# Kernel optimization log

Measured on AMD Instinct MI355X. Metric: run time of the kernel, lower is better.

## Reference

```python
import jax, jax.numpy as jnp
import numpy as np

T, D, H, N = 2048, 2048, 32, 64
DW, DA, DV, DG = 64, 64, 32, 128


def _ln(x, w, b, eps):
    mu = x.mean(-1, keepdims=True)
    var = ((x - mu) ** 2).mean(-1, keepdims=True)
    return (x - mu) * jax.lax.rsqrt(var + eps) * w + b


def setup_inputs() -> dict:
    key = jax.random.key(0)
    ks = iter(jax.random.split(key, 40))

    def rn(shape, s=0.02):
        return jax.random.normal(next(ks), shape, dtype=jnp.float32) * s

    def ru(shape):
        return jax.random.uniform(next(ks), shape, dtype=jnp.float32)

    return dict(
        x=rn((T, D), 1.0),
        state1=rn((1, D), 1.0),
        state2=rn((H, N, N), 0.1),
        v_first=rn((T, D), 1.0),
        ln1_w=jnp.ones((D,), jnp.float32),
        ln1_b=jnp.zeros((D,), jnp.float32),
        x_r=ru((D,)), x_w=ru((D,)), x_k=ru((D,)),
        x_v=ru((D,)), x_a=ru((D,)), x_g=ru((D,)),
        W_r=rn((D, D)), W_k=rn((D, D)), W_v=rn((D, D)), W_o=rn((D, D)),
        w1=rn((D, DW)), w2=rn((DW, D)), w0=rn((D,), 0.5),
        a1=rn((D, DA)), a2=rn((DA, D)), a0=rn((D,), 0.5),
        v1=rn((D, DV)), v2=rn((DV, D)), v0=rn((D,), 0.5),
        g1=rn((D, DG)), g2=rn((DG, D)),
        k_k=rn((D,), 0.5), k_a=rn((D,), 0.5), r_k=rn((D,), 0.5),
        ln_x_w=jnp.ones((D,), jnp.float32),
        ln_x_b=jnp.zeros((D,), jnp.float32),
    )


def reference(x, state1, state2, v_first, ln1_w, ln1_b,
              x_r, x_w, x_k, x_v, x_a, x_g,
              W_r, W_k, W_v, W_o,
              w1, w2, w0, a1, a2, a0, v1, v2, v0, g1, g2,
              k_k, k_a, r_k, ln_x_w, ln_x_b):
    # ln1 + token shift
    xn = _ln(x, ln1_w, ln1_b, 1e-5)                      # [T, D]
    sx = jnp.concatenate([state1, xn[:-1]], axis=0) - xn  # shifted - x
    xr = xn + sx * x_r
    xw = xn + sx * x_w
    xk = xn + sx * x_k
    xv = xn + sx * x_v
    xa = xn + sx * x_a
    xg = xn + sx * x_g

    r = xr @ W_r.T
    # decay: w = exp(-0.606531 * sigmoid(w0 + tanh(xw@w1)@w2))
    w = jnp.exp(-0.606531 * jax.nn.sigmoid(jnp.tanh(xw @ w1) @ w2 + w0))
    k = xk @ W_k.T
    v = xv @ W_v.T
    a = jax.nn.sigmoid(xa @ a1 @ a2 + a0)
    g = jax.nn.sigmoid(xg @ g1) @ g2
    # layer_id != 0: blend with v_first via v-lora
    v = v + (v_first - v) * jax.nn.sigmoid(xv @ v1 @ v2 + v0)

    kh = (k * k_k).reshape(T, H, N)
    kk = kh / (jnp.linalg.norm(kh, axis=-1, keepdims=True) + 1e-6)  # l2norm per head
    k = k * (1.0 + (a - 1.0) * k_a)

    rh = r.reshape(T, H, N)
    wh = w.reshape(T, H, N)
    khh = k.reshape(T, H, N)
    vh = v.reshape(T, H, N)
    ab = kk * a.reshape(T, H, N)  # b input to wkv

    def step(S, t):
        r_t, w_t, k_t, v_t, kk_t, ab_t = t
        sa = jnp.einsum('hij,hj->hi', S, -kk_t)  # state @ a (a = -kk column)
        S = (S * w_t[:, None, :]
             + sa[:, :, None] * ab_t[:, None, :]
             + v_t[:, :, None] * k_t[:, None, :])
        return S, jnp.einsum('hij,hj->hi', S, r_t)

    state2_out, xo = jax.lax.scan(step, state2, (rh, wh, khh, vh, kk, ab))  # xo: [T,H,N]

    # per-head layernorm (ln_x, eps=0.00064), then full-width affine
    xo = _ln(xo, jnp.float32(1.0), jnp.float32(0.0), 0.00064)
    xo = xo.reshape(T, D) * ln_x_w + ln_x_b
    # r_k bonus term
    bonus = ((rh * khh * r_k.reshape(H, N)).sum(-1, keepdims=True) * vh).reshape(T, D)
    xo = (xo + bonus) * g
    out = x + xo @ W_o.T
    return out, xn[-1:], state2_out
```

## Files before the change

### kernel.cpp

```cpp
#include <hip/hip_runtime.h>

#define Tn 2048
#define Dn 2048
#define Hn 32
#define Cn 32
#define NCH (Tn / Cn)

typedef float f32x4 __attribute__((ext_vector_type(4)));
typedef __bf16 bf16x8 __attribute__((ext_vector_type(8)));
typedef __bf16 bf16x4 __attribute__((ext_vector_type(4)));

template <int CTRL>
__device__ __forceinline__ float dpp_add(float x) {
  int xi = __builtin_bit_cast(int, x);
  int sh = __builtin_amdgcn_update_dpp(0, xi, CTRL, 0xf, 0xf, true);
  return x + __builtin_bit_cast(float, sh);
}
__device__ __forceinline__ float rdlane(float x, int l) {
  int xi = __builtin_bit_cast(int, x);
  return __builtin_bit_cast(float, __builtin_amdgcn_readlane(xi, l));
}
__device__ __forceinline__ float waveSum(float v) {
  v = dpp_add<0x111>(v);
  v = dpp_add<0x112>(v);
  v = dpp_add<0x114>(v);
  v = dpp_add<0x118>(v);
  return (rdlane(v, 15) + rdlane(v, 31)) + (rdlane(v, 47) + rdlane(v, 63));
}

__device__ __forceinline__ float sigm(float x) { return 1.f / (1.f + expf(-x)); }

__device__ __forceinline__ void gl_lds16(const void* g, void* l) {
  __builtin_amdgcn_global_load_lds(
      (__attribute__((address_space(1))) void*)(g),
      (__attribute__((address_space(3))) void*)(l), 16, 0, 0);
}

__device__ __forceinline__ void bar_lgkm() {
  asm volatile("s_waitcnt lgkmcnt(0)" ::: "memory");
  __builtin_amdgcn_s_barrier();
}

__device__ __forceinline__ f32x4 mfma16(const __bf16* a, const __bf16* b, f32x4 acc) {
  return __builtin_amdgcn_mfma_f32_16x16x32_bf16(
      *(const bf16x8*)a, *(const bf16x8*)b, acc, 0, 0, 0);
}


__global__ __launch_bounds__(256) void castw3_kernel(
    const float* __restrict__ A, const float* __restrict__ B,
    const float* __restrict__ C, __bf16* __restrict__ o0,
    __bf16* __restrict__ o1, __bf16* __restrict__ o2) {
  const int z = blockIdx.y;
  const float* src = z == 0 ? A : (z == 1 ? B : C);
  __bf16* dst = z == 0 ? o0 : (z == 1 ? o1 : o2);
  const size_t i4 = (size_t)blockIdx.x * 256 + threadIdx.x;
  f32x4 v = *(const f32x4*)(src + i4 * 4);
  bf16x4 o;
  o[0] = (__bf16)v[0]; o[1] = (__bf16)v[1]; o[2] = (__bf16)v[2]; o[3] = (__bf16)v[3];
  ((bf16x4*)dst)[i4] = o;
}

__global__ __launch_bounds__(256) void cast1_kernel(
    const float* __restrict__ src, __bf16* __restrict__ dst) {
  const size_t i4 = (size_t)blockIdx.x * 256 + threadIdx.x;
  f32x4 v = *(const f32x4*)(src + i4 * 4);
  bf16x4 o;
  o[0] = (__bf16)v[0]; o[1] = (__bf16)v[1]; o[2] = (__bf16)v[2]; o[3] = (__bf16)v[3];
  ((bf16x4*)dst)[i4] = o;
}

__global__ __launch_bounds__(256) void castT_kernel(
    const float* __restrict__ w2, const float* __restrict__ a2,
    const float* __restrict__ v2, const float* __restrict__ g2,
    __bf16* __restrict__ w2T, __bf16* __restrict__ a2T,
    __bf16* __restrict__ v2T, __bf16* __restrict__ g2T) {
  const int i = blockIdx.x;
  const int k = threadIdx.x;
  if (k < 128) {
    w2T[(size_t)i * 128 + k] = (k < 64) ? (__bf16)w2[(size_t)k * Dn + i] : (__bf16)0.f;
    a2T[(size_t)i * 128 + k] = (k < 64) ? (__bf16)a2[(size_t)k * Dn + i] : (__bf16)0.f;
    v2T[(size_t)i * 128 + k] = (k < 32) ? (__bf16)v2[(size_t)k * Dn + i] : (__bf16)0.f;
    g2T[(size_t)i * 128 + k] = (__bf16)g2[(size_t)k * Dn + i];
  }
}

__global__ __launch_bounds__(256) void castU_kernel(
    const float* __restrict__ w1, const float* __restrict__ a1,
    const float* __restrict__ v1, const float* __restrict__ g1,
    __bf16* __restrict__ uwT, __bf16* __restrict__ uaT,
    __bf16* __restrict__ uvT, __bf16* __restrict__ ugT) {
  const int z = blockIdx.y;
  const float* src = z == 0 ? w1 : (z == 1 ? a1 : (z == 2 ? v1 : g1));
  __bf16* dst = z == 0 ? uwT : (z == 1 ? uaT : (z == 2 ? uvT : ugT));
  const int R = z == 0 ? 64 : (z == 1 ? 64 : (z == 2 ? 32 : 128));
  const int d = blockIdx.x;
  const int k = threadIdx.x;
  if (k < 128)
    dst[(size_t)k * Dn + d] = (k < R) ? (__bf16)src[(size_t)d * R + k] : (__bf16)0.f;
}


__global__ __launch_bounds__(256) void ln_kernel(
    const float* __restrict__ x, const float* __restrict__ lw,
    const float* __restrict__ lb, __bf16* __restrict__ xn,
    float* __restrict__ xn_last) {
  __shared__ float red[8];
  const int t = blockIdx.x, tid = threadIdx.x;
  const int lane = tid & 63, wv = tid >> 6;
  const float* xr = x + (size_t)t * Dn;
  float v[8];
  float s = 0.f;
#pragma unroll
  for (int c = 0; c < 8; ++c) { v[c] = xr[tid + c * 256]; s += v[c]; }
  s = waveSum(s);
  if (lane == 0) red[wv] = s;
  __syncthreads();
  const float mu = (red[0] + red[1] + red[2] + red[3]) * (1.f / (float)Dn);
  float q = 0.f;
#pragma unroll
  for (int c = 0; c < 8; ++c) { float d0 = v[c] - mu; q += d0 * d0; }
  q = waveSum(q);
  if (lane == 0) red[4 + wv] = q;
  __syncthreads();
  const float var = (red[4] + red[5] + red[6] + red[7]) * (1.f / (float)Dn);
  const float rstd = rsqrtf(var + 1e-5f);
#pragma unroll
  for (int c = 0; c < 8; ++c) {
    const int d = tid + c * 256;
    const float y = (v[c] - mu) * rstd * lw[d] + lb[d];
    xn[(size_t)t * Dn + d] = (__bf16)y;
    if (t == Tn - 1) xn_last[d] = y;
  }
}


__global__ __launch_bounds__(256) void mix_kernel(
    const __bf16* __restrict__ xn, const float* __restrict__ state1,
    const float* __restrict__ cr, const float* __restrict__ cw,
    const float* __restrict__ ck, const float* __restrict__ cv,
    const float* __restrict__ ca, const float* __restrict__ cg,
    __bf16* __restrict__ br, __bf16* __restrict__ bw, __bf16* __restrict__ bk,
    __bf16* __restrict__ bv, __bf16* __restrict__ ba, __bf16* __restrict__ bg) {
  const size_t i4 = (size_t)blockIdx.x * 256 + threadIdx.x;
  const int t = (int)(i4 >> 9);
  const int d = (int)(i4 & 511) * 4;
  const bf16x4 cb = ((const bf16x4*)xn)[i4];
  f32x4 cur;
#pragma unroll
  for (int e = 0; e < 4; ++e) cur[e] = (float)cb[e];
  f32x4 prv;
  if (t == 0) {
    prv = *(const f32x4*)(state1 + d);
  } else {
    const bf16x4 pb = ((const bf16x4*)xn)[i4 - 512];
#pragma unroll
    for (int e = 0; e < 4; ++e) prv[e] = (float)pb[e];
  }
  const f32x4 sx = prv - cur;
  auto mix1 = [&](const float* c, __bf16* o) {
    const f32x4 cc = *(const f32x4*)(c + d);
    bf16x4 ob;
#pragma unroll
    for (int e = 0; e < 4; ++e) ob[e] = (__bf16)(cur[e] + sx[e] * cc[e]);
    ((bf16x4*)o)[i4] = ob;
  };
  mix1(cr, br); mix1(cw, bw); mix1(ck, bk);
  mix1(cv, bv); mix1(ca, ba); mix1(cg, bg);
}


__device__ __forceinline__ void gemm_tile(const __bf16* __restrict__ A,
                                          const __bf16* __restrict__ B,
                                          int K, int row0, int col0,
                                          f32x4 (&acc)[4][4]) {
  __shared__ __attribute__((aligned(16))) __bf16 As[4096];
  __shared__ __attribute__((aligned(16))) __bf16 Bs[4096];
  const int tid = threadIdx.x;
  const int lane = tid & 63, wid = tid >> 6;
  const int wm = (wid >> 1) * 64, wn = (wid & 1) * 64;
  const int lr = lane & 15, lk = (lane >> 4) * 8;
  for (int kt = 0; kt < K; kt += 32) {
#pragma unroll
    for (int it = 0; it < 2; ++it) {
      const int L = it * 256 + tid;
      const int rr = L >> 2, kc = (L & 3) * 8;
      const int lb = (it * 256 + wid * 64) * 8;
      gl_lds16(A + (size_t)(row0 + rr) * K + (kt + kc), &As[lb]);
      gl_lds16(B + (size_t)(col0 + rr) * K + (kt + kc), &Bs[lb]);
    }
    __syncthreads();
    bf16x8 af[4], bfv[4];
#pragma unroll
    for (int mf = 0; mf < 4; ++mf)
      af[mf] = *(const bf16x8*)&As[(wm + mf * 16 + lr) * 32 + lk];
#pragma unroll
    for (int nf = 0; nf < 4; ++nf)
      bfv[nf] = *(const bf16x8*)&Bs[(wn + nf * 16 + lr) * 32 + lk];
#pragma unroll
    for (int mf = 0; mf < 4; ++mf)
#pragma unroll
      for (int nf = 0; nf < 4; ++nf)
        acc[mf][nf] = __builtin_amdgcn_mfma_f32_16x16x32_bf16(
            af[mf], bfv[nf], acc[mf][nf], 0, 0, 0);
    __syncthreads();
  }
}

__global__ __launch_bounds__(256) void gemm37_kernel(
    const __bf16* __restrict__ A0, const __bf16* __restrict__ A1,
    const __bf16* __restrict__ A2, const __bf16* __restrict__ B0,
    const __bf16* __restrict__ B1, const __bf16* __restrict__ B2,
    __bf16* __restrict__ C0, __bf16* __restrict__ C1, __bf16* __restrict__ C2,
    const __bf16* __restrict__ Aw, const __bf16* __restrict__ Aa,
    const __bf16* __restrict__ Av, const __bf16* __restrict__ Ag,
    const __bf16* __restrict__ Bw, const __bf16* __restrict__ Ba,
    const __bf16* __restrict__ Bv, const __bf16* __restrict__ Bg,
    __bf16* __restrict__ Cw, __bf16* __restrict__ Ca,
    __bf16* __restrict__ Cv, __bf16* __restrict__ Cg) {
  const int z = blockIdx.z;
  if (z >= 3 && blockIdx.y != 0) return;
  const __bf16* A; const __bf16* B; __bf16* C;
  switch (z) {
    case 0: A = A0; B = B0; C = C0; break;
    case 1: A = A1; B = B1; C = C1; break;
    case 2: A = A2; B = B2; C = C2; break;
    case 3: A = Aw; B = Bw; C = Cw; break;
    case 4: A = Aa; B = Ba; C = Ca; break;
    case 5: A = Av; B = Bv; C = Cv; break;
    default: A = Ag; B = Bg; C = Cg; break;
  }
  const int row0 = blockIdx.x * 128, col0 = (z < 3) ? blockIdx.y * 128 : 0;
  const int ldc = (z < 3) ? Dn : 128;
  f32x4 acc[4][4] = {};
  gemm_tile(A, B, Dn, row0, col0, acc);
  const int lane = threadIdx.x & 63, wid = threadIdx.x >> 6;
  const int wm = (wid >> 1) * 64, wn = (wid & 1) * 64;
#pragma unroll
  for (int mf = 0; mf < 4; ++mf) {
    const int r0 = row0 + wm + mf * 16 + ((lane >> 4) << 2);
#pragma unroll
    for (int nf = 0; nf < 4; ++nf) {
      const int c0 = col0 + wn + nf * 16 + (lane & 15);
#pragma unroll
      for (int rg = 0; rg < 4; ++rg) {
        float val = acc[mf][nf][rg];
        if (z == 3)      val = tanhf(val);
        else if (z == 6) val = sigm(val);
        C[(size_t)(r0 + rg) * ldc + c0] = (__bf16)val;
      }
    }
  }
}

__global__ __launch_bounds__(256) void gemm_s2_kernel(
    const __bf16* __restrict__ Aw, const __bf16* __restrict__ Aa,
    const __bf16* __restrict__ Av, const __bf16* __restrict__ Ag,
    const __bf16* __restrict__ Bw, const __bf16* __restrict__ Ba,
    const __bf16* __restrict__ Bv, const __bf16* __restrict__ Bg,
    const float* __restrict__ w0, const float* __restrict__ a0,
    const float* __restrict__ v0, __bf16* __restrict__ Cw,
    __bf16* __restrict__ Ca, __bf16* __restrict__ Cv, __bf16* __restrict__ Cg) {
  const int z = blockIdx.z;
  const __bf16* A = z == 0 ? Aw : (z == 1 ? Aa : (z == 2 ? Av : Ag));
  const __bf16* B = z == 0 ? Bw : (z == 1 ? Ba : (z == 2 ? Bv : Bg));
  const float* bias = z == 0 ? w0 : (z == 1 ? a0 : (z == 2 ? v0 : (const float*)0));
  __bf16* C = z == 0 ? Cw : (z == 1 ? Ca : (z == 2 ? Cv : Cg));
  const int row0 = blockIdx.x * 128, col0 = blockIdx.y * 128;
  f32x4 acc[4][4] = {};
  gemm_tile(A, B, 128, row0, col0, acc);
  const int lane = threadIdx.x & 63, wid = threadIdx.x >> 6;
  const int wm = (wid >> 1) * 64, wn = (wid & 1) * 64;
#pragma unroll
  for (int mf = 0; mf < 4; ++mf) {
    const int r0 = row0 + wm + mf * 16 + ((lane >> 4) << 2);
#pragma unroll
    for (int nf = 0; nf < 4; ++nf) {
      const int c0 = col0 + wn + nf * 16 + (lane & 15);
#pragma unroll
      for (int rg = 0; rg < 4; ++rg) {
        float val = acc[mf][nf][rg];
        if (z == 0)      val = expf(-0.606531f * sigm(val + bias[c0]));
        else if (z < 3)  val = sigm(val + bias[c0]);
        C[(size_t)(r0 + rg) * Dn + c0] = (__bf16)val;
      }
    }
  }
}

__global__ __launch_bounds__(256) void gemm_wo_kernel(
    const __bf16* __restrict__ A, const __bf16* __restrict__ B,
    const float* __restrict__ xres, float* __restrict__ C) {
  const int row0 = blockIdx.x * 128, col0 = blockIdx.y * 128;
  f32x4 acc[4][4] = {};
  gemm_tile(A, B, Dn, row0, col0, acc);
  const int lane = threadIdx.x & 63, wid = threadIdx.x >> 6;
  const int wm = (wid >> 1) * 64, wn = (wid & 1) * 64;
#pragma unroll
  for (int mf = 0; mf < 4; ++mf) {
    const int r0 = row0 + wm + mf * 16 + ((lane >> 4) << 2);
#pragma unroll
    for (int nf = 0; nf < 4; ++nf) {
      const int c0 = col0 + wn + nf * 16 + (lane & 15);
#pragma unroll
      for (int rg = 0; rg < 4; ++rg)
        C[(size_t)(r0 + rg) * Dn + c0] =
            acc[mf][nf][rg] + xres[(size_t)(r0 + rg) * Dn + c0];
    }
  }
}


__global__ __launch_bounds__(256) void prep_kernel(
    const __bf16* __restrict__ r, __bf16* __restrict__ k, __bf16* __restrict__ v,
    const __bf16* __restrict__ a, const __bf16* __restrict__ vb,
    const float* __restrict__ v_first, const float* __restrict__ k_k,
    const float* __restrict__ k_a, const float* __restrict__ r_k,
    __bf16* __restrict__ kk_out, __bf16* __restrict__ ab_out,
    float* __restrict__ dot_out) {
  const int t = blockIdx.x;
  const int lane = threadIdx.x & 63, wv = threadIdx.x >> 6;
#pragma unroll 1
  for (int c = 0; c < 8; ++c) {
    const int d = c * 256 + wv * 64 + lane;
    const size_t idx = (size_t)t * Dn + d;
    const float kvv = (float)k[idx];
    const float kh = kvv * k_k[d];
    const float nrm = sqrtf(waveSum(kh * kh)) + 1e-6f;
    const float kkv = kh / nrm;
    const float av = (float)a[idx];
    float vv = (float)v[idx];
    vv = vv + (v_first[idx] - vv) * (float)vb[idx];
    const float kfv = kvv * (1.f + (av - 1.f) * k_a[d]);
    const float dt = waveSum((float)r[idx] * kfv * r_k[d]);
    kk_out[idx] = (__bf16)kkv;
    ab_out[idx] = (__bf16)(kkv * av);
    k[idx] = (__bf16)kfv;
    v[idx] = (__bf16)vv;
    if (lane == 0) dot_out[t * Hn + (d >> 6)] = dt;
  }
}


__global__ __launch_bounds__(256) void chunkA_kernel(
    const __bf16* __restrict__ wd, const __bf16* __restrict__ kk,
    const __bf16* __restrict__ ab, const __bf16* __restrict__ kf,
    const __bf16* __restrict__ r,
    __bf16* __restrict__ PAg, __bf16* __restrict__ Rtil,
    __bf16* __restrict__ BhatT, __bf16* __restrict__ KhatT,
    __bf16* __restrict__ PKg,
    __bf16* __restrict__ Gbg, __bf16* __restrict__ Gkg,
    float* __restrict__ WCg) {
  const int c = blockIdx.x, h = blockIdx.y;
  const int tid = threadIdx.x;
  const int lane = tid & 63, wid = tid >> 6;
  const int lr = lane & 15, lg = lane >> 4, lk = lg * 8;
  __shared__ __attribute__((aligned(16))) __bf16 A_l[32][72];
  __shared__ __attribute__((aligned(16))) __bf16 B_l[32][72], K_l[32][72], R_l[32][72];
  __shared__ __attribute__((aligned(16))) __bf16 At_t[64][40];
  __shared__ float W_l[33][64];
  __shared__ __attribute__((aligned(16))) __bf16 Mn[32][40], Mt[32][40], Mkat[32][40];
  __shared__ __attribute__((aligned(16))) __bf16 Pa[32][40], Pb[32][40];
  __shared__ __attribute__((aligned(16))) __bf16 Tn_[32][40], Tt_[32][40];
  __shared__ __attribute__((aligned(16))) __bf16 Un_[32][40], Ut_[32][40];

  const size_t rowbase = (size_t)(c * Cn) * Dn + (size_t)h * 64;
  const int tt = tid >> 3, j0 = (tid & 7) * 8;
  const size_t g = rowbase + (size_t)tt * Dn + j0;
  *(bf16x8*)&A_l[tt][j0] = *(const bf16x8*)(wd + g);
  __syncthreads();
  if (tid < 64) {
    const int j = tid;
    float cur = 1.f;
    W_l[0][j] = 1.f;
    for (int t = 0; t < Cn; ++t) {
      cur *= (float)A_l[t][j];
      W_l[t + 1][j] = cur;
    }
    WCg[((size_t)c * Hn + h) * 64 + j] = cur;
  }
  __syncthreads();
  {
    bf16x8 kkv = *(const bf16x8*)(kk + g);
    bf16x8 abv = *(const bf16x8*)(ab + g);
    bf16x8 kv  = *(const bf16x8*)(kf + g);
    bf16x8 rv  = *(const bf16x8*)(r + g);
    bf16x8 oa, ob, ok, orr;
    const size_t tb = ((size_t)c * Hn + h) * 2048;
#pragma unroll
    for (int e = 0; e < 8; ++e) {
      const int j = j0 + e;
      const float Wexc = W_l[tt][j], Winc = W_l[tt + 1][j], WC = W_l[32][j];
      const float inv = 1.f / Winc;
      const float at = -(float)kkv[e] * Wexc;
      const float bt = (float)abv[e] * inv;
      const float kt = (float)kv[e] * inv;
      const float rt = (float)rv[e] * Winc;
      oa[e] = (__bf16)at; ob[e] = (__bf16)bt; ok[e] = (__bf16)kt;
      orr[e] = (__bf16)rt;
      At_t[j][tt] = (__bf16)at;
      BhatT[tb + (size_t)j * 32 + tt] = (__bf16)(bt * WC);
      KhatT[tb + (size_t)j * 32 + tt] = (__bf16)(kt * WC);
    }
    *(bf16x8*)&A_l[tt][j0] = oa;
    *(bf16x8*)&B_l[tt][j0] = ob;
    *(bf16x8*)&K_l[tt][j0] = ok;
    *(bf16x8*)&R_l[tt][j0] = orr;
    *(bf16x8*)(Rtil + g) = orr;
  }
  __syncthreads();
  const size_t matbase = ((size_t)c * Hn + h) * (Cn * Cn);
  {
    const __bf16 (*Ax)[72] = (wid < 2) ? A_l : R_l;
    const __bf16 (*Bx)[72] = ((wid & 1) == 0) ? B_l : K_l;
#pragma unroll
    for (int tile = 0; tile < 4; ++tile) {
      const int tm = (tile >> 1) * 16, tn = (tile & 1) * 16;
      f32x4 acc = {};
      acc = mfma16(&Ax[tm + lr][lk], &Bx[tn + lr][lk], acc);
      acc = mfma16(&Ax[tm + lr][32 + lk], &Bx[tn + lr][32 + lk], acc);
      const int col = tn + lr;
#pragma unroll
      for (int e = 0; e < 4; ++e) {
        const int row = tm + lg * 4 + e;
        if (wid == 0) {
          const __bf16 v = (__bf16)((col < row) ? acc[e] : 0.f);
          Mn[row][col] = v; Mt[col][row] = v;
        } else if (wid == 1) {
          Mkat[col][row] = (__bf16)((col < row) ? acc[e] : 0.f);
        } else if (wid == 2) {
          Gbg[matbase + row * 32 + col] = (__bf16)((col <= row) ? acc[e] : 0.f);
        } else {
          Gkg[matbase + row * 32 + col] = (__bf16)((col <= row) ? acc[e] : 0.f);
        }
      }
    }
  }
  __syncthreads();
  for (int rep = 0; rep < 4; ++rep) {
    const int id = rep * 256 + tid;
    const int t = id >> 5, ta = id & 31;
    Pa[t][ta] = (__bf16)((float)Mn[t][ta] + (t == ta ? 1.f : 0.f));
  }
  __syncthreads();
  const int tm = (wid >> 1) * 16, tn = (wid & 1) * 16;
  auto sq = [&](__bf16 (*Dn_)[40], __bf16 (*Dt_)[40],
                __bf16 (*Xn)[40], __bf16 (*Xt)[40]) {
    f32x4 acc = {};
    acc = mfma16(&Xn[tm + lr][lk], &Xt[tn + lr][lk], acc);
    const int col = tn + lr;
#pragma unroll
    for (int e = 0; e < 4; ++e) {
      const int row = tm + lg * 4 + e;
      const __bf16 v = (__bf16)acc[e];
      Dn_[row][col] = v; Dt_[col][row] = v;
    }
    __syncthreads();
  };
  auto pup = [&](__bf16 (*Dn_)[40], __bf16 (*Pn)[40], __bf16 (*Tt)[40]) {
    f32x4 acc;
    const int col = tn + lr;
#pragma unroll
    for (int e = 0; e < 4; ++e) acc[e] = (float)Pn[tm + lg * 4 + e][col];
    acc = mfma16(&Pn[tm + lr][lk], &Tt[tn + lr][lk], acc);
#pragma unroll
    for (int e = 0; e < 4; ++e) Dn_[tm + lg * 4 + e][col] = (__bf16)acc[e];
    __syncthreads();
  };
  sq(Tn_, Tt_, Mn, Mt);
  pup(Pb, Pa, Tt_);
  sq(Un_, Ut_, Tn_, Tt_);
  pup(Pa, Pb, Ut_);
  sq(Tn_, Tt_, Un_, Ut_);
  pup(Pb, Pa, Tt_);
  sq(Un_, Ut_, Tn_, Tt_);
  pup(Pa, Pb, Ut_);
  {
    f32x4 acc = {};
    acc = mfma16(&Pa[tm + lr][lk], &Mkat[tn + lr][lk], acc);
    const int col = tn + lr;
#pragma unroll
    for (int e = 0; e < 4; ++e)
      PKg[matbase + (tm + lg * 4 + e) * 32 + col] = (__bf16)acc[e];
  }
#pragma unroll
  for (int half = 0; half < 2; ++half) {
    const int jn = (wid & 1) * 16 + half * 32;
    f32x4 acc = {};
    acc = mfma16(&Pa[tm + lr][lk], &At_t[jn + lr][lk], acc);
    const int col = jn + lr;
#pragma unroll
    for (int e = 0; e < 4; ++e)
      PAg[rowbase + (size_t)(tm + lg * 4 + e) * Dn + col] = (__bf16)acc[e];
  }
}


__global__ __launch_bounds__(256) void vt_kernel(
    const __bf16* __restrict__ vbuf, __bf16* __restrict__ Vt) {
  const int c = blockIdx.x, h = blockIdx.y;
  __shared__ __bf16 tile[32][72];
  const int tid = threadIdx.x;
  {
    const int t = tid >> 3, i0 = (tid & 7) * 8;
    *(bf16x8*)&tile[t][i0] =
        *(const bf16x8*)(vbuf + (size_t)(c * Cn + t) * Dn + h * 64 + i0);
  }
  __syncthreads();
  {
    const int i = tid >> 2, t0 = (tid & 3) * 8;
    bf16x8 o;
#pragma unroll
    for (int e = 0; e < 8; ++e) o[e] = tile[t0 + e][i];
    *(bf16x8*)(Vt + ((size_t)c * Hn + h) * 2048 + (size_t)i * 32 + t0) = o;
  }
}


__global__ __launch_bounds__(256) void chunkB_kernel(
    const __bf16* __restrict__ PAg, const __bf16* __restrict__ Rtil,
    const __bf16* __restrict__ BhatT, const __bf16* __restrict__ KhatT,
    const __bf16* __restrict__ PKg,
    const __bf16* __restrict__ Gbg, const __bf16* __restrict__ Gkg,
    const float* __restrict__ WCg, const __bf16* __restrict__ Vt,
    const float* __restrict__ st_in, __bf16* __restrict__ xo,
    float* __restrict__ st_out) {
  const int b = blockIdx.x;
  const int xcd = b & 7, rest = b >> 3;
  const int h = xcd * 4 + (rest & 3);
  const int io = (rest >> 2) * 32;
  const int tid = threadIdx.x;
  const int lane = tid & 63, wid = tid >> 6;
  const int lr = lane & 15, lg = lane >> 4;
  const int lk = lg * 8;

  __shared__ __attribute__((aligned(16))) float S_l[32][68];
  __shared__ __attribute__((aligned(16))) __bf16 Sb_l[32][72];
  __shared__ __attribute__((aligned(16))) __bf16 PA_l[32][72], R_l[32][72];
  __shared__ __attribute__((aligned(16))) __bf16 BhT_l[64][40], KhT_l[64][40];
  __shared__ __attribute__((aligned(16))) __bf16 Vt_l[32][40];
  __shared__ __attribute__((aligned(16))) __bf16 PK_l[32][40];
  __shared__ __attribute__((aligned(16))) __bf16 Gb_l[32][40], Gk_l[32][40];
  __shared__ __attribute__((aligned(16))) __bf16 SA_l[32][40];
  __shared__ float WC_l[64];

  {
    const int i = tid >> 3, j0 = (tid & 7) * 8;
    const float* src = st_in + (size_t)h * 4096 + (size_t)(io + i) * 64 + j0;
    *(f32x4*)&S_l[i][j0] = *(const f32x4*)src;
    *(f32x4*)&S_l[i][j0 + 4] = *(const f32x4*)(src + 4);
  }

  bf16x8 rPA, rR, rBh, rKh;
  bf16x4 rV, rPK, rGb, rGk;
  float rWC = 0.f;

  auto load_regs = [&](int c) {
    const size_t rb = (size_t)(c * Cn) * Dn + (size_t)h * 64;
    {
      const int t = tid >> 3, j0 = (tid & 7) * 8;
      rPA = *(const bf16x8*)(PAg + rb + (size_t)t * Dn + j0);
      rR  = *(const bf16x8*)(Rtil + rb + (size_t)t * Dn + j0);
    }
    const size_t tb = ((size_t)c * Hn + h) * 2048;
    {
      const int jj = tid >> 2, t0 = (tid & 3) * 8;
      rBh = *(const bf16x8*)(BhatT + tb + (size_t)jj * 32 + t0);
      rKh = *(const bf16x8*)(KhatT + tb + (size_t)jj * 32 + t0);
    }
    {
      const int i = tid >> 3, t0 = (tid & 7) * 4;
      rV = *(const bf16x4*)(Vt + tb + (size_t)(io + i) * 32 + t0);
    }
    const size_t mb = ((size_t)c * Hn + h) * 1024 + (size_t)tid * 4;
    rPK = *(const bf16x4*)(PKg + mb);
    rGb = *(const bf16x4*)(Gbg + mb);
    rGk = *(const bf16x4*)(Gkg + mb);
    if (tid < 64) rWC = WCg[((size_t)c * Hn + h) * 64 + tid];
  };
  auto store_lds = [&]() {
    {
      const int t = tid >> 3, j0 = (tid & 7) * 8;
      *(bf16x8*)&PA_l[t][j0] = rPA;
      *(bf16x8*)&R_l[t][j0] = rR;
    }
    {
      const int jj = tid >> 2, t0 = (tid & 3) * 8;
      *(bf16x8*)&BhT_l[jj][t0] = rBh;
      *(bf16x8*)&KhT_l[jj][t0] = rKh;
    }
    {
      const int i = tid >> 3, t0 = (tid & 7) * 4;
      *(bf16x4*)&Vt_l[i][t0] = rV;
    }
    {
      const int t = tid >> 3, u0 = (tid & 7) * 4;
      *(bf16x4*)&PK_l[t][u0] = rPK;
      *(bf16x4*)&Gb_l[t][u0] = rGb;
      *(bf16x4*)&Gk_l[t][u0] = rGk;
    }
    if (tid < 64) WC_l[tid] = rWC;
  };
  auto sb_refresh = [&]() {
    const int i = tid >> 3, j0 = (tid & 7) * 8;
    bf16x8 o;
#pragma unroll
    for (int e = 0; e < 8; ++e) o[e] = (__bf16)S_l[i][j0 + e];
    *(bf16x8*)&Sb_l[i][j0] = o;
  };

  load_regs(0);
  store_lds();
  sb_refresh();
  bar_lgkm();

  const int tm = (wid >> 1) * 16, tn = (wid & 1) * 16;

#pragma unroll 1
  for (int c = 0; c < NCH; ++c) {
    load_regs(c + 1 < NCH ? c + 1 : c);
    {
      f32x4 acc = {};
      acc = mfma16(&PA_l[tm + lr][lk], &Sb_l[tn + lr][lk], acc);
      acc = mfma16(&PA_l[tm + lr][32 + lk], &Sb_l[tn + lr][32 + lk], acc);
      acc = mfma16(&PK_l[tm + lr][lk], &Vt_l[tn + lr][lk], acc);
      bf16x4 o;
#pragma unroll
      for (int e = 0; e < 4; ++e) o[e] = (__bf16)acc[e];
      *(bf16x4*)&SA_l[tn + lr][tm + lg * 4] = o;
    }
    bar_lgkm();
    {
      f32x4 acc = {};
      acc = mfma16(&Gb_l[tm + lr][lk], &SA_l[tn + lr][lk], acc);
      acc = mfma16(&Gk_l[tm + lr][lk], &Vt_l[tn + lr][lk], acc);
      acc = mfma16(&R_l[tm + lr][lk], &Sb_l[tn + lr][lk], acc);
      acc = mfma16(&R_l[tm + lr][32 + lk], &Sb_l[tn + lr][32 + lk], acc);
      const int ig = h * 64 + io + tn + lr;
#pragma unroll
      for (int e = 0; e < 4; ++e)
        xo[(size_t)(c * Cn + tm + lg * 4 + e) * Dn + ig] = (__bf16)acc[e];
    }
#pragma unroll
    for (int tt = 0; tt < 2; ++tt) {
      const int tix = wid + tt * 4;
      const int im = (tix & 1) * 16, jn = (tix >> 1) * 16;
      const float wc = WC_l[jn + lr];
      f32x4 acc;
#pragma unroll
      for (int e = 0; e < 4; ++e) acc[e] = S_l[im + lg * 4 + e][jn + lr] * wc;
      acc = mfma16(&SA_l[im + lr][lk], &BhT_l[jn + lr][lk], acc);
      acc = mfma16(&Vt_l[im + lr][lk], &KhT_l[jn + lr][lk], acc);
#pragma unroll
      for (int e = 0; e < 4; ++e) S_l[im + lg * 4 + e][jn + lr] = acc[e];
    }
    bar_lgkm();
    store_lds();
    sb_refresh();
    bar_lgkm();
  }
  {
    const int i = tid >> 3, j0 = (tid & 7) * 8;
    float* dst = st_out + (size_t)h * 4096 + (size_t)(io + i) * 64 + j0;
    *(f32x4*)dst = *(const f32x4*)&S_l[i][j0];
    *(f32x4*)(dst + 4) = *(const f32x4*)&S_l[i][j0 + 4];
  }
}


__global__ __launch_bounds__(256) void post_kernel(
    const __bf16* __restrict__ xo, const __bf16* __restrict__ v,
    const __bf16* __restrict__ g, const float* __restrict__ dot,
    const float* __restrict__ lnw, const float* __restrict__ lnb,
    __bf16* __restrict__ out) {
  const int t = blockIdx.x;
  const int lane = threadIdx.x & 63, wv = threadIdx.x >> 6;
#pragma unroll 1
  for (int c = 0; c < 8; ++c) {
    const int d = c * 256 + wv * 64 + lane;
    const size_t idx = (size_t)t * Dn + d;
    const float val = (float)xo[idx];
    const float mu = waveSum(val) * (1.f / 64.f);
    const float ctr = val - mu;
    const float var = waveSum(ctr * ctr) * (1.f / 64.f);
    float y = ctr * rsqrtf(var + 0.00064f);
    y = y * lnw[d] + lnb[d];
    const float res = (y + dot[t * Hn + (d >> 6)] * (float)v[idx]) * (float)g[idx];
    out[idx] = (__bf16)res;
  }
}


extern "C" void kernel_launch(void* const* d_in, const int* in_sizes, int n_in,
                              void* d_out, int out_size, void* d_ws, size_t ws_size,
                              hipStream_t stream) {
  (void)in_sizes; (void)n_in; (void)out_size; (void)ws_size;
  const float* x       = (const float*)d_in[0];
  const float* state1  = (const float*)d_in[1];
  const float* state2  = (const float*)d_in[2];
  const float* v_first = (const float*)d_in[3];
  const float* ln1_w   = (const float*)d_in[4];
  const float* ln1_b   = (const float*)d_in[5];
  const float* x_r     = (const float*)d_in[6];
  const float* x_w     = (const float*)d_in[7];
  const float* x_k     = (const float*)d_in[8];
  const float* x_v     = (const float*)d_in[9];
  const float* x_a     = (const float*)d_in[10];
  const float* x_g     = (const float*)d_in[11];
  const float* W_r     = (const float*)d_in[12];
  const float* W_k     = (const float*)d_in[13];
  const float* W_v     = (const float*)d_in[14];
  const float* W_o     = (const float*)d_in[15];
  const float* w1      = (const float*)d_in[16];
  const float* w2      = (const float*)d_in[17];
  const float* w0      = (const float*)d_in[18];
  const float* a1      = (const float*)d_in[19];
  const float* a2      = (const float*)d_in[20];
  const float* a0      = (const float*)d_in[21];
  const float* v1      = (const float*)d_in[22];
  const float* v2      = (const float*)d_in[23];
  const float* v0      = (const float*)d_in[24];
  const float* g1      = (const float*)d_in[25];
  const float* g2      = (const float*)d_in[26];
  const float* k_k     = (const float*)d_in[27];
  const float* k_a     = (const float*)d_in[28];
  const float* r_k     = (const float*)d_in[29];
  const float* lnx_w   = (const float*)d_in[30];
  const float* lnx_b   = (const float*)d_in[31];

  char* p = (char*)d_ws;
  const size_t MB = 1ull << 20;
  __bf16* xn    = (__bf16*)(p + 0 * MB);
  __bf16* PAg   = (__bf16*)(p + 0 * MB);
  __bf16* xr_b  = (__bf16*)(p + 8 * MB);
  __bf16* Wo_b  = (__bf16*)(p + 8 * MB);
  __bf16* xw_b  = (__bf16*)(p + 16 * MB);
  __bf16* wdec  = (__bf16*)(p + 16 * MB);
  __bf16* xo_b  = (__bf16*)(p + 16 * MB);
  __bf16* xk_b  = (__bf16*)(p + 24 * MB);
  __bf16* abuf  = (__bf16*)(p + 24 * MB);
  __bf16* Rtil  = (__bf16*)(p + 24 * MB);
  __bf16* xv_b  = (__bf16*)(p + 32 * MB);
  __bf16* vbl   = (__bf16*)(p + 32 * MB);
  __bf16* BhatT = (__bf16*)(p + 32 * MB);
  __bf16* xa_b  = (__bf16*)(p + 40 * MB);
  __bf16* gbuf  = (__bf16*)(p + 40 * MB);
  __bf16* xg_b  = (__bf16*)(p + 48 * MB);
  __bf16* kkbuf = (__bf16*)(p + 48 * MB);
  __bf16* xobuf = (__bf16*)(p + 48 * MB);
  __bf16* Wr_b  = (__bf16*)(p + 56 * MB);
  __bf16* abbuf = (__bf16*)(p + 56 * MB);
  __bf16* Wk_b  = (__bf16*)(p + 64 * MB);
  __bf16* KhatT = (__bf16*)(p + 64 * MB);
  __bf16* Wv_b  = (__bf16*)(p + 72 * MB);
  __bf16* PKg   = (__bf16*)(p + 72 * MB);
  __bf16* rbuf  = (__bf16*)(p + 80 * MB);
  __bf16* kbuf  = (__bf16*)(p + 88 * MB);
  __bf16* Vt    = (__bf16*)(p + 88 * MB);
  __bf16* vbuf  = (__bf16*)(p + 96 * MB);
  __bf16* Gbg   = (__bf16*)(p + 104 * MB);
  __bf16* Gkg   = (__bf16*)(p + 108 * MB);
  char* q = p + 112 * MB;
  __bf16* yw  = (__bf16*)q; q += (size_t)Tn * 128 * 2;
  __bf16* ya  = (__bf16*)q; q += (size_t)Tn * 128 * 2;
  __bf16* yv  = (__bf16*)q; q += (size_t)Tn * 128 * 2;
  __bf16* yg  = (__bf16*)q; q += (size_t)Tn * 128 * 2;
  __bf16* uwT = (__bf16*)q; q += (size_t)128 * Dn * 2;
  __bf16* uaT = (__bf16*)q; q += (size_t)128 * Dn * 2;
  __bf16* uvT = (__bf16*)q; q += (size_t)128 * Dn * 2;
  __bf16* ugT = (__bf16*)q; q += (size_t)128 * Dn * 2;
  __bf16* w2T = (__bf16*)q; q += (size_t)Dn * 128 * 2;
  __bf16* a2T = (__bf16*)q; q += (size_t)Dn * 128 * 2;
  __bf16* v2T = (__bf16*)q; q += (size_t)Dn * 128 * 2;
  __bf16* g2T = (__bf16*)q; q += (size_t)Dn * 128 * 2;
  float*  dot = (float*)q;  q += (size_t)Tn * Hn * 4;
  float*  WCg = (float*)q;  q += (size_t)NCH * Hn * 64 * 4;

  float* out     = (float*)d_out;
  float* out_xnl = out + (size_t)Tn * Dn;
  float* out_st  = out_xnl + Dn;

  castw3_kernel<<<dim3(4096, 3), 256, 0, stream>>>(W_r, W_k, W_v, Wr_b, Wk_b, Wv_b);
  castT_kernel<<<2048, 256, 0, stream>>>(w2, a2, v2, g2, w2T, a2T, v2T, g2T);
  castU_kernel<<<dim3(2048, 4), 256, 0, stream>>>(w1, a1, v1, g1, uwT, uaT, uvT, ugT);
  ln_kernel<<<2048, 256, 0, stream>>>(x, ln1_w, ln1_b, xn, out_xnl);
  mix_kernel<<<4096, 256, 0, stream>>>(xn, state1, x_r, x_w, x_k, x_v, x_a, x_g,
                                       xr_b, xw_b, xk_b, xv_b, xa_b, xg_b);
  gemm37_kernel<<<dim3(16, 16, 7), 256, 0, stream>>>(
      xr_b, xk_b, xv_b, Wr_b, Wk_b, Wv_b, rbuf, kbuf, vbuf,
      xw_b, xa_b, xv_b, xg_b, uwT, uaT, uvT, ugT, yw, ya, yv, yg);
  cast1_kernel<<<4096, 256, 0, stream>>>(W_o, Wo_b);
  gemm_s2_kernel<<<dim3(16, 16, 4), 256, 0, stream>>>(
      yw, ya, yv, yg, w2T, a2T, v2T, g2T, w0, a0, v0, wdec, abuf, vbl, gbuf);
  prep_kernel<<<2048, 256, 0, stream>>>(rbuf, kbuf, vbuf, abuf, vbl, v_first,
                                        k_k, k_a, r_k, kkbuf, abbuf, dot);
  chunkA_kernel<<<dim3(NCH, Hn), 256, 0, stream>>>(
      wdec, kkbuf, abbuf, kbuf, rbuf,
      PAg, Rtil, BhatT, KhatT, PKg, Gbg, Gkg, WCg);
  vt_kernel<<<dim3(NCH, Hn), 256, 0, stream>>>(vbuf, Vt);
  chunkB_kernel<<<64, 256, 0, stream>>>(
      PAg, Rtil, BhatT, KhatT, PKg, Gbg, Gkg, WCg, Vt,
      state2, xobuf, out_st);
  post_kernel<<<2048, 256, 0, stream>>>(xobuf, vbuf, gbuf, dot, lnx_w, lnx_b, xo_b);
  gemm_wo_kernel<<<dim3(16, 16), 256, 0, stream>>>(xo_b, Wo_b, x, out);
}
```

Before: 381.4 us.

## Fuse layernorm with token-shift mix, merge weight casts, swizzle GEMM blocks across XCDs

Merges the layernorm and token-shift mix kernels into one kernel. Each block recomputes the previous row's layernorm statistics itself, so the bf16 xn buffer is never written or read back. The two small weight-transpose cast kernels become one launch, which saves a kernel launch. A block-index swizzle groups GEMM tiles per XCD in the square projection GEMMs and the output GEMM to improve L2 reuse. The trade-off is that every row of x is read twice, and the mix now works in fp32 rather than on bf16-rounded xn.

```diff
diff --git a/kernel.cpp b/kernel.cpp
--- a/kernel.cpp
+++ b/kernel.cpp
@@ -70,103 +70,90 @@
   ((bf16x4*)dst)[i4] = o;
 }
 
-__global__ __launch_bounds__(256) void castT_kernel(
+__global__ __launch_bounds__(256) void castTU_kernel(
     const float* __restrict__ w2, const float* __restrict__ a2,
     const float* __restrict__ v2, const float* __restrict__ g2,
     __bf16* __restrict__ w2T, __bf16* __restrict__ a2T,
-    __bf16* __restrict__ v2T, __bf16* __restrict__ g2T) {
-  const int i = blockIdx.x;
+    __bf16* __restrict__ v2T, __bf16* __restrict__ g2T,
+    const float* __restrict__ w1, const float* __restrict__ a1,
+    const float* __restrict__ v1, const float* __restrict__ g1,
+    __bf16* __restrict__ uwT, __bf16* __restrict__ uaT,
+    __bf16* __restrict__ uvT, __bf16* __restrict__ ugT) {
   const int k = threadIdx.x;
-  if (k < 128) {
+  if (k >= 128) return;
+  const int y = blockIdx.y;
+  if (y == 0) {
+    const int i = blockIdx.x;
     w2T[(size_t)i * 128 + k] = (k < 64) ? (__bf16)w2[(size_t)k * Dn + i] : (__bf16)0.f;
     a2T[(size_t)i * 128 + k] = (k < 64) ? (__bf16)a2[(size_t)k * Dn + i] : (__bf16)0.f;
     v2T[(size_t)i * 128 + k] = (k < 32) ? (__bf16)v2[(size_t)k * Dn + i] : (__bf16)0.f;
     g2T[(size_t)i * 128 + k] = (__bf16)g2[(size_t)k * Dn + i];
-  }
-}
-
-__global__ __launch_bounds__(256) void castU_kernel(
-    const float* __restrict__ w1, const float* __restrict__ a1,
-    const float* __restrict__ v1, const float* __restrict__ g1,
-    __bf16* __restrict__ uwT, __bf16* __restrict__ uaT,
-    __bf16* __restrict__ uvT, __bf16* __restrict__ ugT) {
-  const int z = blockIdx.y;
-  const float* src = z == 0 ? w1 : (z == 1 ? a1 : (z == 2 ? v1 : g1));
-  __bf16* dst = z == 0 ? uwT : (z == 1 ? uaT : (z == 2 ? uvT : ugT));
-  const int R = z == 0 ? 64 : (z == 1 ? 64 : (z == 2 ? 32 : 128));
-  const int d = blockIdx.x;
-  const int k = threadIdx.x;
-  if (k < 128)
+  } else {
+    const int z = y - 1;
+    const float* src = z == 0 ? w1 : (z == 1 ? a1 : (z == 2 ? v1 : g1));
+    __bf16* dst = z == 0 ? uwT : (z == 1 ? uaT : (z == 2 ? uvT : ugT));
+    const int R = z == 0 ? 64 : (z == 1 ? 64 : (z == 2 ? 32 : 128));
+    const int d = blockIdx.x;
     dst[(size_t)k * Dn + d] = (k < R) ? (__bf16)src[(size_t)d * R + k] : (__bf16)0.f;
-}
-
-
-__global__ __launch_bounds__(256) void ln_kernel(
-    const float* __restrict__ x, const float* __restrict__ lw,
-    const float* __restrict__ lb, __bf16* __restrict__ xn,
-    float* __restrict__ xn_last) {
-  __shared__ float red[8];
-  const int t = blockIdx.x, tid = threadIdx.x;
-  const int lane = tid & 63, wv = tid >> 6;
-  const float* xr = x + (size_t)t * Dn;
-  float v[8];
-  float s = 0.f;
-#pragma unroll
-  for (int c = 0; c < 8; ++c) { v[c] = xr[tid + c * 256]; s += v[c]; }
-  s = waveSum(s);
-  if (lane == 0) red[wv] = s;
-  __syncthreads();
-  const float mu = (red[0] + red[1] + red[2] + red[3]) * (1.f / (float)Dn);
-  float q = 0.f;
-#pragma unroll
-  for (int c = 0; c < 8; ++c) { float d0 = v[c] - mu; q += d0 * d0; }
-  q = waveSum(q);
-  if (lane == 0) red[4 + wv] = q;
-  __syncthreads();
-  const float var = (red[4] + red[5] + red[6] + red[7]) * (1.f / (float)Dn);
-  const float rstd = rsqrtf(var + 1e-5f);
-#pragma unroll
-  for (int c = 0; c < 8; ++c) {
-    const int d = tid + c * 256;
-    const float y = (v[c] - mu) * rstd * lw[d] + lb[d];
-    xn[(size_t)t * Dn + d] = (__bf16)y;
-    if (t == Tn - 1) xn_last[d] = y;
-  }
-}
-
-
-__global__ __launch_bounds__(256) void mix_kernel(
-    const __bf16* __restrict__ xn, const float* __restrict__ state1,
+  }
+}
+
+
+__global__ __launch_bounds__(256) void lnmix_kernel(
+    const float* __restrict__ x, const float* __restrict__ state1,
+    const float* __restrict__ lw, const float* __restrict__ lb,
     const float* __restrict__ cr, const float* __restrict__ cw,
     const float* __restrict__ ck, const float* __restrict__ cv,
     const float* __restrict__ ca, const float* __restrict__ cg,
     __bf16* __restrict__ br, __bf16* __restrict__ bw, __bf16* __restrict__ bk,
-    __bf16* __restrict__ bv, __bf16* __restrict__ ba, __bf16* __restrict__ bg) {
-  const size_t i4 = (size_t)blockIdx.x * 256 + threadIdx.x;
-  const int t = (int)(i4 >> 9);
-  const int d = (int)(i4 & 511) * 4;
-  const bf16x4 cb = ((const bf16x4*)xn)[i4];
-  f32x4 cur;
-#pragma unroll
-  for (int e = 0; e < 4; ++e) cur[e] = (float)cb[e];
-  f32x4 prv;
-  if (t == 0) {
-    prv = *(const f32x4*)(state1 + d);
-  } else {
-    const bf16x4 pb = ((const bf16x4*)xn)[i4 - 512];
-#pragma unroll
-    for (int e = 0; e < 4; ++e) prv[e] = (float)pb[e];
-  }
-  const f32x4 sx = prv - cur;
-  auto mix1 = [&](const float* c, __bf16* o) {
-    const f32x4 cc = *(const f32x4*)(c + d);
-    bf16x4 ob;
-#pragma unroll
-    for (int e = 0; e < 4; ++e) ob[e] = (__bf16)(cur[e] + sx[e] * cc[e]);
-    ((bf16x4*)o)[i4] = ob;
-  };
-  mix1(cr, br); mix1(cw, bw); mix1(ck, bk);
-  mix1(cv, bv); mix1(ca, ba); mix1(cg, bg);
+    __bf16* __restrict__ bv, __bf16* __restrict__ ba, __bf16* __restrict__ bg,
+    float* __restrict__ xn_last) {
+  __shared__ float red[16];
+  const int t = blockIdx.x, tid = threadIdx.x;
+  const int lane = tid & 63, wv = tid >> 6;
+  const float* xc = x + (size_t)t * Dn;
+  const float* xp = x + (size_t)(t - 1) * Dn;
+  float vc[8], vp[8];
+  float sc = 0.f, sp = 0.f;
+#pragma unroll
+  for (int c = 0; c < 8; ++c) {
+    vc[c] = xc[tid + c * 256]; sc += vc[c];
+    vp[c] = (t > 0) ? xp[tid + c * 256] : 0.f; sp += vp[c];
+  }
+  sc = waveSum(sc); sp = waveSum(sp);
+  if (lane == 0) { red[wv] = sc; red[8 + wv] = sp; }
+  __syncthreads();
+  const float mu_c = (red[0] + red[1] + red[2] + red[3]) * (1.f / (float)Dn);
+  const float mu_p = (red[8] + red[9] + red[10] + red[11]) * (1.f / (float)Dn);
+  float qc = 0.f, qp = 0.f;
+#pragma unroll
+  for (int c = 0; c < 8; ++c) {
+    float d0 = vc[c] - mu_c; qc += d0 * d0;
+    float d1 = vp[c] - mu_p; qp += d1 * d1;
+  }
+  qc = waveSum(qc); qp = waveSum(qp);
+  if (lane == 0) { red[4 + wv] = qc; red[12 + wv] = qp; }
+  __syncthreads();
+  const float var_c = (red[4] + red[5] + red[6] + red[7]) * (1.f / (float)Dn);
+  const float var_p = (red[12] + red[13] + red[14] + red[15]) * (1.f / (float)Dn);
+  const float rstd_c = rsqrtf(var_c + 1e-5f);
+  const float rstd_p = rsqrtf(var_p + 1e-5f);
+#pragma unroll
+  for (int c = 0; c < 8; ++c) {
+    const int d = tid + c * 256;
+    const size_t idx = (size_t)t * Dn + d;
+    const float lwd = lw[d], lbd = lb[d];
+    const float ync = (vc[c] - mu_c) * rstd_c * lwd + lbd;
+    const float ynp = (t > 0) ? ((vp[c] - mu_p) * rstd_p * lwd + lbd) : state1[d];
+    const float sx = ynp - ync;
+    br[idx] = (__bf16)(ync + sx * cr[d]);
+    bw[idx] = (__bf16)(ync + sx * cw[d]);
+    bk[idx] = (__bf16)(ync + sx * ck[d]);
+    bv[idx] = (__bf16)(ync + sx * cv[d]);
+    ba[idx] = (__bf16)(ync + sx * ca[d]);
+    bg[idx] = (__bf16)(ync + sx * cg[d]);
+    if (t == Tn - 1) xn_last[d] = ync;
+  }
 }
 
 
@@ -205,6 +192,13 @@
             af[mf], bfv[nf], acc[mf][nf], 0, 0, 0);
     __syncthreads();
   }
+}
+
+__device__ __forceinline__ void xcd_swz16(int& bx, int& by) {
+  const int lid = bx + (by << 4);
+  const int xcd = lid & 7, idx = lid >> 3;
+  bx = ((xcd & 3) << 2) + (idx & 3);
+  by = ((xcd >> 2) << 3) + (idx >> 2);
 }
 
 __global__ __launch_bounds__(256) void gemm37_kernel(
@@ -230,7 +224,9 @@
     case 5: A = Av; B = Bv; C = Cv; break;
     default: A = Ag; B = Bg; C = Cg; break;
   }
-  const int row0 = blockIdx.x * 128, col0 = (z < 3) ? blockIdx.y * 128 : 0;
+  int bx = blockIdx.x, by = blockIdx.y;
+  if (z < 3) xcd_swz16(bx, by);
+  const int row0 = bx * 128, col0 = (z < 3) ? by * 128 : 0;
   const int ldc = (z < 3) ? Dn : 128;
   f32x4 acc[4][4] = {};
   gemm_tile(A, B, Dn, row0, col0, acc);
@@ -291,7 +287,9 @@
 __global__ __launch_bounds__(256) void gemm_wo_kernel(
     const __bf16* __restrict__ A, const __bf16* __restrict__ B,
     const float* __restrict__ xres, float* __restrict__ C) {
-  const int row0 = blockIdx.x * 128, col0 = blockIdx.y * 128;
+  int bx = blockIdx.x, by = blockIdx.y;
+  xcd_swz16(bx, by);
+  const int row0 = bx * 128, col0 = by * 128;
   f32x4 acc[4][4] = {};
   gemm_tile(A, B, Dn, row0, col0, acc);
   const int lane = threadIdx.x & 63, wid = threadIdx.x >> 6;
@@ -642,8 +640,8 @@
         xo[(size_t)(c * Cn + tm + lg * 4 + e) * Dn + ig] = (__bf16)acc[e];
     }
 #pragma unroll
-    for (int tt = 0; tt < 2; ++tt) {
-      const int tix = wid + tt * 4;
+    for (int tt2 = 0; tt2 < 2; ++tt2) {
+      const int tix = wid + tt2 * 4;
       const int im = (tix & 1) * 16, jn = (tix >> 1) * 16;
       const float wc = WC_l[jn + lr];
       f32x4 acc;
@@ -730,7 +728,6 @@
 
   char* p = (char*)d_ws;
   const size_t MB = 1ull << 20;
-  __bf16* xn    = (__bf16*)(p + 0 * MB);
   __bf16* PAg   = (__bf16*)(p + 0 * MB);
   __bf16* xr_b  = (__bf16*)(p + 8 * MB);
   __bf16* Wo_b  = (__bf16*)(p + 8 * MB);
@@ -781,11 +778,12 @@
   float* out_st  = out_xnl + Dn;
 
   castw3_kernel<<<dim3(4096, 3), 256, 0, stream>>>(W_r, W_k, W_v, Wr_b, Wk_b, Wv_b);
-  castT_kernel<<<2048, 256, 0, stream>>>(w2, a2, v2, g2, w2T, a2T, v2T, g2T);
-  castU_kernel<<<dim3(2048, 4), 256, 0, stream>>>(w1, a1, v1, g1, uwT, uaT, uvT, ugT);
-  ln_kernel<<<2048, 256, 0, stream>>>(x, ln1_w, ln1_b, xn, out_xnl);
-  mix_kernel<<<4096, 256, 0, stream>>>(xn, state1, x_r, x_w, x_k, x_v, x_a, x_g,
-                                       xr_b, xw_b, xk_b, xv_b, xa_b, xg_b);
+  castTU_kernel<<<dim3(2048, 5), 256, 0, stream>>>(
+      w2, a2, v2, g2, w2T, a2T, v2T, g2T,
+      w1, a1, v1, g1, uwT, uaT, uvT, ugT);
+  lnmix_kernel<<<2048, 256, 0, stream>>>(
+      x, state1, ln1_w, ln1_b, x_r, x_w, x_k, x_v, x_a, x_g,
+      xr_b, xw_b, xk_b, xv_b, xa_b, xg_b, out_xnl);
   gemm37_kernel<<<dim3(16, 16, 7), 256, 0, stream>>>(
       xr_b, xk_b, xv_b, Wr_b, Wk_b, Wv_b, rbuf, kbuf, vbuf,
       xw_b, xa_b, xv_b, xg_b, uwT, uaT, uvT, ugT, yw, ya, yv, yg);
```

After: 372.6 us. 2.3% less time.
